# Kernel optimization log

Hardware: AMD Instinct MI355X
Metric: run time of the kernel (lower is better)

Reference implementation:

```python
import jax, jax.numpy as jnp
import numpy as np

N_NODES = 50000
N_EDGES = 800000
HIDDEN = 128
NUM_LAYERS = 3
NEG_SLOPE = 0.2  # PyG GATConv default leaky_relu slope


def setup_inputs() -> dict:
    key = jax.random.key(0)
    ks = jax.random.split(key, 10)
    d = HIDDEN
    glorot = 1.0 / np.sqrt(d)
    inp = {
        "x": jax.random.normal(ks[0], (N_NODES, d), dtype=jnp.float32),
        "edge_index": jax.random.randint(ks[1], (2, N_EDGES), 0, N_NODES, dtype=jnp.int32),
        "edge_mask": jax.random.uniform(ks[2], (N_EDGES,), dtype=jnp.float32),
        # GATConv params (heads=1)
        "W_gat": jax.random.normal(ks[3], (d, d), dtype=jnp.float32) * glorot,
        "a_src": jax.random.normal(ks[4], (d,), dtype=jnp.float32) * glorot,
        "a_dst": jax.random.normal(ks[5], (d,), dtype=jnp.float32) * glorot,
        "b_gat": jnp.zeros((d,), dtype=jnp.float32),
        # Stacked GCNConv params
        "W_gcn": jax.random.normal(ks[6], (NUM_LAYERS, d, d), dtype=jnp.float32) * glorot,
        "b_gcn": jnp.zeros((NUM_LAYERS, d), dtype=jnp.float32),
    }
    return inp


def _seg_softmax(e, seg, n):
    m = jax.ops.segment_max(e, seg, num_segments=n)
    p = jnp.exp(e - m[seg])
    s = jax.ops.segment_sum(p, seg, num_segments=n)
    return p / s[seg]


def reference(x, edge_index, edge_mask, W_gat, a_src, a_dst, b_gat, W_gcn, b_gcn):
    N = x.shape[0]
    loops = jnp.arange(N, dtype=edge_index.dtype)
    src = jnp.concatenate([edge_index[0], loops])  # [E+N] with self loops
    dst = jnp.concatenate([edge_index[1], loops])

    # --- GATConv (heads=1, add_self_loops=True); edge_attr ignored (edge_dim=None) ---
    xp = x @ W_gat                                      # [N, d]
    e = jax.nn.leaky_relu((xp @ a_src)[src] + (xp @ a_dst)[dst], NEG_SLOPE)
    alpha = _seg_softmax(e, dst, N)                     # segment softmax over incoming edges
    h = jax.ops.segment_sum(alpha[:, None] * xp[src], dst, num_segments=N) + b_gat

    # --- GCN normalization with edge_mask as edge_weight (self-loop weight = 1) ---
    w = jnp.concatenate([edge_mask, jnp.ones((N,), dtype=edge_mask.dtype)])
    deg = jax.ops.segment_sum(w, dst, num_segments=N)
    dinv = jnp.where(deg > 0, jax.lax.rsqrt(jnp.maximum(deg, 1e-12)), 0.0)
    norm = dinv[src] * w * dinv[dst]                    # [E+N]

    outs = [h]
    for l in range(NUM_LAYERS):
        z = outs[-1] @ W_gcn[l]                         # [N, d]
        z = jax.ops.segment_sum(norm[:, None] * z[src], dst, num_segments=N) + b_gcn[l]
        outs.append(jax.nn.relu(z))

    # JumpingKnowledge 'max': elementwise max over layer outputs
    return jnp.max(jnp.stack(outs, axis=0), axis=0)
```

## Files before the change

kernel.cpp:

```cpp
#include <hip/hip_runtime.h>

#define HIDDEN 128
#define NEG_SLOPE 0.2f
#define P_SORT 256

typedef unsigned short ushort_t;
typedef __attribute__((ext_vector_type(8))) short short8;
typedef __attribute__((ext_vector_type(4))) float floatx4;

static inline size_t align_up(size_t x, size_t a){ return (x + a - 1) & ~(a - 1); }

__device__ __forceinline__ ushort_t f2b(float f){
  unsigned u = __float_as_uint(f);
  unsigned r = (u + 0x7FFFu + ((u >> 16) & 1u)) >> 16;
  return (ushort_t)r;
}

__device__ __forceinline__ void fma8(float* acc, uint4 v, float a){
  acc[0] += a * __uint_as_float(v.x << 16);
  acc[1] += a * __uint_as_float(v.x & 0xFFFF0000u);
  acc[2] += a * __uint_as_float(v.y << 16);
  acc[3] += a * __uint_as_float(v.y & 0xFFFF0000u);
  acc[4] += a * __uint_as_float(v.z << 16);
  acc[5] += a * __uint_as_float(v.z & 0xFFFF0000u);
  acc[6] += a * __uint_as_float(v.w << 16);
  acc[7] += a * __uint_as_float(v.w & 0xFFFF0000u);
}

__device__ __forceinline__ uint4 pack8(const float* f){
  uint4 u;
  u.x = (unsigned)f2b(f[0]) | ((unsigned)f2b(f[1]) << 16);
  u.y = (unsigned)f2b(f[2]) | ((unsigned)f2b(f[3]) << 16);
  u.z = (unsigned)f2b(f[4]) | ((unsigned)f2b(f[5]) << 16);
  u.w = (unsigned)f2b(f[6]) | ((unsigned)f2b(f[7]) << 16);
  return u;
}


__global__ __launch_bounds__(256) void k_b1cnt(const int* __restrict__ dst,
                                               int* __restrict__ bcnt,
                                               int E, int epb, int nbkt){
  __shared__ unsigned c[256];
  int t = threadIdx.x;
  c[t] = 0;
  __syncthreads();
  int e0 = blockIdx.x * epb;
  int e1 = min(E, e0 + epb);
  for (int e = e0 + t; e < e1; e += 256) atomicAdd(&c[dst[e] >> 8], 1u);
  __syncthreads();
  if (t < nbkt) bcnt[t * P_SORT + blockIdx.x] = (int)c[t];
}

__global__ void k_scan1(const int* __restrict__ in, int* __restrict__ incl,
                        int* __restrict__ blockSums, int M){
  __shared__ int sd[256];
  int t = threadIdx.x;
  int i = blockIdx.x*256 + t;
  int v = (i < M) ? in[i] : 0;
  sd[t] = v; __syncthreads();
  for (int off = 1; off < 256; off <<= 1){
    int add = (t >= off) ? sd[t-off] : 0;
    __syncthreads();
    sd[t] += add;
    __syncthreads();
  }
  if (i < M) incl[i] = sd[t];
  if (t == 255) blockSums[blockIdx.x] = sd[255];
}

__global__ void k_scan2(const int* __restrict__ blockSums, int* __restrict__ blockOffs, int nb){
  __shared__ int sd[256];
  __shared__ int carry;
  int t = threadIdx.x;
  if (t == 0) carry = 0;
  __syncthreads();
  for (int base = 0; base < nb; base += 256){
    int i = base + t;
    int v = (i < nb) ? blockSums[i] : 0;
    sd[t] = v; __syncthreads();
    for (int off = 1; off < 256; off <<= 1){
      int add = (t >= off) ? sd[t-off] : 0;
      __syncthreads();
      sd[t] += add;
      __syncthreads();
    }
    if (i < nb) blockOffs[i] = carry + sd[t] - v;
    __syncthreads();
    if (t == 0) carry += sd[255];
    __syncthreads();
  }
}

__global__ __launch_bounds__(256) void k_b1place(const int* __restrict__ src,
                                                 const int* __restrict__ dst,
                                                 const float* __restrict__ w,
                                                 const int* __restrict__ incl,
                                                 const int* __restrict__ bcnt,
                                                 const int* __restrict__ blockOffs,
                                                 int2* __restrict__ tpw,
                                                 int E, int epb, int nbkt){
  __shared__ int base_[256];
  __shared__ unsigned c[256];
  int t = threadIdx.x;
  c[t] = 0;
  if (t < nbkt){
    int idx = t * P_SORT + blockIdx.x;
    base_[t] = incl[idx] - bcnt[idx] + blockOffs[t];
  }
  __syncthreads();
  int e0 = blockIdx.x * epb;
  int e1 = min(E, e0 + epb);
  for (int e = e0 + t; e < e1; e += 256){
    int d = dst[e];
    int b = d >> 8;
    unsigned r = atomicAdd(&c[b], 1u);
    int pos = base_[b] + (int)r;
    tpw[pos] = make_int2((int)((unsigned)src[e] | ((unsigned)(d & 255) << 16)),
                         __float_as_int(w[e]));
  }
}

__global__ __launch_bounds__(256) void k_b2(const int2* __restrict__ tpw,
                                            const int* __restrict__ blockOffs,
                                            int2* __restrict__ col_sw,
                                            int* __restrict__ rowp,
                                            float* __restrict__ dinv,
                                            int N, int E, int nbkt){
  __shared__ unsigned hcnt[256];
  __shared__ int sd[256];
  __shared__ int lofs[256];
  __shared__ unsigned rcnt[256];
  __shared__ float wsum[256];
  int b = blockIdx.x, t = threadIdx.x;
  int e0 = blockOffs[b];
  int e1 = (b + 1 < nbkt) ? blockOffs[b + 1] : E;
  hcnt[t] = 0; rcnt[t] = 0; wsum[t] = 0.f;
  __syncthreads();
  for (int e = e0 + t; e < e1; e += 256)
    atomicAdd(&hcnt[((unsigned)tpw[e].x >> 16) & 255u], 1u);
  __syncthreads();
  int v = (int)hcnt[t];
  sd[t] = v; __syncthreads();
  for (int off = 1; off < 256; off <<= 1){
    int add = (t >= off) ? sd[t-off] : 0;
    __syncthreads();
    sd[t] += add;
    __syncthreads();
  }
  lofs[t] = sd[t] - v;
  int node = b*256 + t;
  if (node < N) rowp[node] = e0 + sd[t] - v;
  if (b == 0 && t == 0) rowp[N] = E;
  __syncthreads();
  for (int e = e0 + t; e < e1; e += 256){
    int2 pw = tpw[e];
    unsigned dl = ((unsigned)pw.x >> 16) & 255u;
    unsigned r = atomicAdd(&rcnt[dl], 1u);
    int pos = e0 + lofs[dl] + (int)r;
    col_sw[pos] = make_int2((int)((unsigned)pw.x & 0xFFFFu), pw.y);
    atomicAdd(&wsum[dl], __int_as_float(pw.y));
  }
  __syncthreads();
  if (node < N) dinv[node] = rsqrtf(wsum[t] + 1.0f);
}


__global__ void k_cast_w(const float* __restrict__ Wg, const float* __restrict__ Wc,
                         ushort_t* __restrict__ Wt){
  int i = blockIdx.x*256 + threadIdx.x;
  int mat = i >> 14, idx = i & 16383;
  int k = idx >> 7, n = idx & 127;
  float v = (mat == 0) ? Wg[idx] : Wc[(mat-1)*16384 + idx];
  Wt[mat*16384 + n*128 + k] = f2b(v);
}

template<int DOTS>
__global__ __launch_bounds__(256) void k_gemm(const void* __restrict__ Ain,
                                              const ushort_t* __restrict__ Wt,
                                              ushort_t* __restrict__ C,
                                              const float* __restrict__ a_src,
                                              const float* __restrict__ a_dst,
                                              const float* __restrict__ dinv,
                                              float2* __restrict__ attr,
                                              float* __restrict__ sdst, int M){
  int wave = threadIdx.x >> 6, l = threadIdx.x & 63;
  int q = l >> 4, lm = l & 15;
  int rowBase = blockIdx.x*128 + wave*32;
  floatx4 acc[2][8];
  #pragma unroll
  for (int mt = 0; mt < 2; mt++)
    #pragma unroll
    for (int nt = 0; nt < 8; nt++) acc[mt][nt] = (floatx4){0.f,0.f,0.f,0.f};

  #pragma unroll
  for (int kc = 0; kc < 4; kc++){
    int k0 = kc*32 + q*8;
    short8 a[2];
    #pragma unroll
    for (int mt = 0; mt < 2; mt++){
      long r = rowBase + mt*16 + lm;
      if (r < M){
        if (DOTS){
          const float* ap = (const float*)Ain + r*128 + k0;
          float4 u = *(const float4*)ap;
          float4 v = *(const float4*)(ap + 4);
          short8 tv;
          tv[0]=(short)f2b(u.x); tv[1]=(short)f2b(u.y); tv[2]=(short)f2b(u.z); tv[3]=(short)f2b(u.w);
          tv[4]=(short)f2b(v.x); tv[5]=(short)f2b(v.y); tv[6]=(short)f2b(v.z); tv[7]=(short)f2b(v.w);
          a[mt] = tv;
        } else {
          a[mt] = *(const short8*)((const ushort_t*)Ain + r*128 + k0);
        }
      } else a[mt] = (short8){0,0,0,0,0,0,0,0};
    }
    #pragma unroll
    for (int nt = 0; nt < 8; nt++){
      short8 b = *(const short8*)(Wt + (nt*16 + lm)*128 + k0);
      acc[0][nt] = __builtin_amdgcn_mfma_f32_16x16x32_bf16(a[0], b, acc[0][nt], 0, 0, 0);
      acc[1][nt] = __builtin_amdgcn_mfma_f32_16x16x32_bf16(a[1], b, acc[1][nt], 0, 0, 0);
    }
  }
  #pragma unroll
  for (int mt = 0; mt < 2; mt++){
    #pragma unroll
    for (int r = 0; r < 4; r++){
      long row = rowBase + mt*16 + q*4 + r;
      if (row < M){
        #pragma unroll
        for (int nt = 0; nt < 8; nt++)
          C[row*128 + nt*16 + lm] = f2b(acc[mt][nt][r]);
      }
    }
  }
  if (DOTS){
    float as8[8], ad8[8];
    #pragma unroll
    for (int nt = 0; nt < 8; nt++){ as8[nt] = a_src[nt*16 + lm]; ad8[nt] = a_dst[nt*16 + lm]; }
    #pragma unroll
    for (int mt = 0; mt < 2; mt++){
      #pragma unroll
      for (int r = 0; r < 4; r++){
        float ps = 0.f, pd = 0.f;
        #pragma unroll
        for (int nt = 0; nt < 8; nt++){
          ps += acc[mt][nt][r] * as8[nt];
          pd += acc[mt][nt][r] * ad8[nt];
        }
        #pragma unroll
        for (int off = 1; off <= 8; off <<= 1){
          ps += __shfl_xor(ps, off, 64);
          pd += __shfl_xor(pd, off, 64);
        }
        long row = rowBase + mt*16 + q*4 + r;
        if (lm == 0 && row < M){
          attr[row] = make_float2(ps, dinv[row]);
          sdst[row] = pd;
        }
      }
    }
  }
}

template<int MODE>
__global__ __launch_bounds__(256) void k_agg(const ushort_t* __restrict__ feat,
                                             const int* __restrict__ rowp,
                                             const int2* __restrict__ col_sw,
                                             int2* __restrict__ col_en,
                                             int2* __restrict__ col_ea,
                                             const float2* __restrict__ attr,
                                             const float* __restrict__ sdst_,
                                             const float* __restrict__ dinv,
                                             const float* __restrict__ bias,
                                             ushort_t* __restrict__ out,
                                             const uint4* __restrict__ j0,
                                             const uint4* __restrict__ j1,
                                             const uint4* __restrict__ j2,
                                             float4* __restrict__ yout, int N){
  int n = blockIdx.x*4 + (threadIdx.x >> 6);
  if (n >= N) return;
  int l = threadIdx.x & 63;
  int rs = rowp[n], re = rowp[n+1];
  float inv = 0.f, pself = 0.f;
  if (MODE == 0){
    float2 an = attr[n];
    float sdd = sdst_[n];
    float es = an.x + sdd;
    es = (es >= 0.f) ? es : NEG_SLOPE*es;
    pself = __expf(es);
    float ps = 0.f;
    for (int j = rs + l; j < re; j += 64){
      int2 sw = col_sw[j];
      float w = __int_as_float(sw.y);
      float2 a = attr[sw.x];
      col_en[j] = make_int2(sw.x, __float_as_int(a.y * w * an.y));
      float ee = a.x + sdd;
      ee = (ee >= 0.f) ? ee : NEG_SLOPE*ee;
      float pe = __expf(ee);
      ps += pe;
      col_ea[j] = make_int2(sw.x, __float_as_int(pe));
    }
    #pragma unroll
    for (int off = 32; off >= 1; off >>= 1) ps += __shfl_xor(ps, off, 64);
    inv = 1.f / (ps + pself);
  }
  const int2* col = (MODE == 0) ? (const int2*)col_ea : (const int2*)col_en;
  int sub = l >> 4, q = l & 15;
  const uint4* f16 = (const uint4*)feat;
  float acc[8] = {0.f,0.f,0.f,0.f,0.f,0.f,0.f,0.f};
  for (int base = rs; base < re; base += 24){
    int2 p[6]; float a[6];
    #pragma unroll
    for (int j = 0; j < 6; j++){
      int e = base + sub + 4*j;
      int cc = min(e, re-1);
      p[j] = col[cc];
      a[j] = (e < re) ? __int_as_float(p[j].y) : 0.f;
    }
    uint4 v[6];
    #pragma unroll
    for (int j = 0; j < 6; j++) v[j] = f16[(size_t)p[j].x*16 + q];
    #pragma unroll
    for (int j = 0; j < 6; j++) fma8(acc, v[j], a[j]);
  }
  #pragma unroll
  for (int j = 0; j < 8; j++){
    acc[j] += __shfl_xor(acc[j], 16, 64);
    acc[j] += __shfl_xor(acc[j], 32, 64);
  }
  if (sub == 0){
    float sc;
    if (MODE == 0){
      #pragma unroll
      for (int j = 0; j < 8; j++) acc[j] *= inv;
      sc = pself * inv;
    } else {
      float di = dinv[n];
      sc = di * di;
    }
    uint4 v = f16[(size_t)n*16 + q];
    fma8(acc, v, sc);
    float4 b0 = ((const float4*)bias)[q*2];
    float4 b1 = ((const float4*)bias)[q*2 + 1];
    acc[0]+=b0.x; acc[1]+=b0.y; acc[2]+=b0.z; acc[3]+=b0.w;
    acc[4]+=b1.x; acc[5]+=b1.y; acc[6]+=b1.z; acc[7]+=b1.w;
    if (MODE >= 1){
      #pragma unroll
      for (int j = 0; j < 8; j++) acc[j] = fmaxf(acc[j], 0.f);
    }
    if (MODE <= 1){
      ((uint4*)out)[(size_t)n*16 + q] = pack8(acc);
    } else {
      size_t qi = (size_t)n*16 + q;
      uint4 a0 = j0[qi], a1 = j1[qi], a2 = j2[qi];
      float m[8];
      #pragma unroll
      for (int k = 0; k < 4; k++){
        unsigned u0 = (&a0.x)[k], u1 = (&a1.x)[k], u2 = (&a2.x)[k];
        float lo = fmaxf(fmaxf(__uint_as_float(u0 << 16), __uint_as_float(u1 << 16)),
                         __uint_as_float(u2 << 16));
        float hi = fmaxf(fmaxf(__uint_as_float(u0 & 0xFFFF0000u), __uint_as_float(u1 & 0xFFFF0000u)),
                         __uint_as_float(u2 & 0xFFFF0000u));
        m[k*2]   = fmaxf(acc[k*2],   lo);
        m[k*2+1] = fmaxf(acc[k*2+1], hi);
      }
      size_t yi = (size_t)n*32 + q*2;
      yout[yi]   = make_float4(m[0], m[1], m[2], m[3]);
      yout[yi+1] = make_float4(m[4], m[5], m[6], m[7]);
    }
  }
}

extern "C" void kernel_launch(void* const* d_in, const int* in_sizes, int n_in,
                              void* d_out, int out_size, void* d_ws, size_t ws_size,
                              hipStream_t stream){
  const float* x      = (const float*)d_in[0];
  const int*   eidx   = (const int*)d_in[1];
  const float* emask  = (const float*)d_in[2];
  const float* W_gat  = (const float*)d_in[3];
  const float* a_src  = (const float*)d_in[4];
  const float* a_dst  = (const float*)d_in[5];
  const float* b_gat  = (const float*)d_in[6];
  const float* W_gcn  = (const float*)d_in[7];
  const float* b_gcn  = (const float*)d_in[8];
  int N = in_sizes[0] / HIDDEN;
  int E = in_sizes[1] / 2;
  const int* src = eidx;
  const int* dst = eidx + E;

  char* p = (char*)d_ws;
  auto carve = [&](size_t bytes)->char*{ char* q = p; p += align_up(bytes, 512); return q; };
  ushort_t* zb   = (ushort_t*)carve((size_t)N*HIDDEN*2);
  ushort_t* h0   = (ushort_t*)carve((size_t)N*HIDDEN*2);
  ushort_t* h1   = (ushort_t*)carve((size_t)N*HIDDEN*2);
  ushort_t* h2   = (ushort_t*)carve((size_t)N*HIDDEN*2);
  ushort_t* Wt   = (ushort_t*)carve((size_t)4*HIDDEN*HIDDEN*2);
  float2* attr   = (float2*)carve((size_t)N*8);
  float* sdst    = (float*)carve((size_t)N*4);
  float* dinv    = (float*)carve((size_t)N*4);
  int*   rowp    = (int*)  carve((size_t)(N+1)*4);
  int2*  col_sw  = (int2*) carve((size_t)E*8);
  int2*  col_en  = (int2*) carve((size_t)E*8);
  int2*  col_ea  = (int2*) carve((size_t)E*8);
  int2*  tpw     = (int2*) carve((size_t)E*8);
  int nbkt = (N + 255) >> 8;
  int M    = nbkt * P_SORT;
  int*   bcnt  = (int*)carve((size_t)M*4);
  int*   incl  = (int*)carve((size_t)M*4);
  int nbs = (M + 255) / 256;
  int*   blockSums = (int*)carve((size_t)nbs*4);
  int*   blockOffs = (int*)carve((size_t)nbs*4);
  (void)ws_size; (void)n_in; (void)out_size;

  int epb = (E + P_SORT - 1) / P_SORT;
  int gb  = (N + 127) / 128;
  int nwb = (N + 3) / 4;

  k_b1cnt  <<<P_SORT, 256, 0, stream>>>(dst, bcnt, E, epb, nbkt);
  k_scan1  <<<nbs, 256, 0, stream>>>(bcnt, incl, blockSums, M);
  k_scan2  <<<1,   256, 0, stream>>>(blockSums, blockOffs, nbs);
  k_b1place<<<P_SORT, 256, 0, stream>>>(src, dst, emask, incl, bcnt, blockOffs,
                                        tpw, E, epb, nbkt);
  k_b2     <<<nbkt, 256, 0, stream>>>(tpw, blockOffs, col_sw, rowp, dinv, N, E, nbkt);

  k_cast_w<<<(4*HIDDEN*HIDDEN)/256, 256, 0, stream>>>(W_gat, W_gcn, Wt);

  k_gemm<1><<<gb, 256, 0, stream>>>((const void*)x, Wt, zb, a_src, a_dst, dinv, attr, sdst, N);

  k_agg<0><<<nwb, 256, 0, stream>>>(zb, rowp, col_sw, col_en, col_ea, attr, sdst,
                                    dinv, b_gat, h0, nullptr, nullptr, nullptr, nullptr, N);

  ushort_t* hs[3] = {h0, h1, h2};
  for (int l = 0; l < 2; l++){
    k_gemm<0><<<gb, 256, 0, stream>>>((const void*)hs[l], Wt + (size_t)(l+1)*HIDDEN*HIDDEN,
                                      zb, a_src, a_dst, dinv, attr, sdst, N);
    k_agg<1><<<nwb, 256, 0, stream>>>(zb, rowp, col_sw, col_en, col_ea, attr, sdst,
                                      dinv, b_gcn + (size_t)l*HIDDEN, hs[l+1],
                                      nullptr, nullptr, nullptr, nullptr, N);
  }
  k_gemm<0><<<gb, 256, 0, stream>>>((const void*)h2, Wt + (size_t)3*HIDDEN*HIDDEN,
                                    zb, a_src, a_dst, dinv, attr, sdst, N);
  k_agg<2><<<nwb, 256, 0, stream>>>(zb, rowp, col_sw, col_en, col_ea, attr, sdst,
                                    dinv, b_gcn + (size_t)2*HIDDEN, nullptr,
                                    (const uint4*)h0, (const uint4*)h1, (const uint4*)h2,
                                    (float4*)d_out, N);
}
```

Baseline: 341.7 us.

## Split edge-softmax into bucket kernel and column-chunk the aggregation grid

Moves GAT edge-score computation out of the layer-0 aggregation into a separate per-bucket kernel that accumulates softmax denominators in shared memory and writes per-node self weights. The aggregation kernels are re-gridded so each block handles one quarter of the feature columns (32 features) for 8 nodes, with 8 edges in flight per half-wave. This spreads gathered rows across four blocks, which may improve cache locality per block and occupancy. Streaming edge lists and outputs now use nontemporal loads and stores. The cost is one extra launch, and each edge list is read four times, once per column chunk.

```diff
diff --git a/kernel.cpp b/kernel.cpp
--- a/kernel.cpp
+++ b/kernel.cpp
@@ -7,6 +7,8 @@
 typedef unsigned short ushort_t;
 typedef __attribute__((ext_vector_type(8))) short short8;
 typedef __attribute__((ext_vector_type(4))) float floatx4;
+typedef __attribute__((ext_vector_type(2))) int intx2;
+typedef __attribute__((ext_vector_type(4))) unsigned uintx4;
 
 static inline size_t align_up(size_t x, size_t a){ return (x + a - 1) & ~(a - 1); }
 
@@ -34,6 +36,27 @@
   u.z = (unsigned)f2b(f[4]) | ((unsigned)f2b(f[5]) << 16);
   u.w = (unsigned)f2b(f[6]) | ((unsigned)f2b(f[7]) << 16);
   return u;
+}
+
+__device__ __forceinline__ int2 ntload2(const int2* p){
+  intx2 v = __builtin_nontemporal_load((const intx2*)p);
+  return make_int2(v.x, v.y);
+}
+__device__ __forceinline__ uint4 ntload4(const uint4* p){
+  uintx4 v = __builtin_nontemporal_load((const uintx4*)p);
+  uint4 r; r.x = v.x; r.y = v.y; r.z = v.z; r.w = v.w; return r;
+}
+__device__ __forceinline__ void ntstore2(int2* p, int2 v){
+  intx2 u; u.x = v.x; u.y = v.y;
+  __builtin_nontemporal_store(u, (intx2*)p);
+}
+__device__ __forceinline__ void ntstore4(uint4* p, uint4 v){
+  uintx4 u; u.x = v.x; u.y = v.y; u.z = v.z; u.w = v.w;
+  __builtin_nontemporal_store(u, (uintx4*)p);
+}
+__device__ __forceinline__ void ntstoref4(float4* p, float a, float b, float c, float d){
+  floatx4 u; u.x = a; u.y = b; u.z = c; u.w = d;
+  __builtin_nontemporal_store(u, (floatx4*)p);
 }
 
 
@@ -157,7 +180,7 @@
     unsigned dl = ((unsigned)pw.x >> 16) & 255u;
     unsigned r = atomicAdd(&rcnt[dl], 1u);
     int pos = e0 + lofs[dl] + (int)r;
-    col_sw[pos] = make_int2((int)((unsigned)pw.x & 0xFFFFu), pw.y);
+    col_sw[pos] = make_int2(pw.x, pw.y);
     atomicAdd(&wsum[dl], __int_as_float(pw.y));
   }
   __syncthreads();
@@ -261,97 +284,120 @@
   }
 }
 
+__global__ __launch_bounds__(256) void k_edge(const int2* __restrict__ col_sw,
+                                              const int* __restrict__ blockOffs,
+                                              const float2* __restrict__ attr,
+                                              const float* __restrict__ sdst_,
+                                              int2* __restrict__ col_en,
+                                              int2* __restrict__ col_ea,
+                                              float2* __restrict__ selfw,
+                                              int N, int E, int nbkt){
+  __shared__ float lps[256];
+  __shared__ float2 lattr[256];
+  __shared__ float lsd[256];
+  int b = blockIdx.x, t = threadIdx.x;
+  int n = b*256 + t;
+  lps[t] = 0.f;
+  if (n < N){ lattr[t] = attr[n]; lsd[t] = sdst_[n]; }
+  else { lattr[t] = make_float2(0.f, 0.f); lsd[t] = 0.f; }
+  __syncthreads();
+  int e0 = blockOffs[b];
+  int e1 = (b + 1 < nbkt) ? blockOffs[b + 1] : E;
+  for (int e = e0 + t; e < e1; e += 256){
+    int2 sw = ntload2(&col_sw[e]);
+    int src = sw.x & 0xFFFF;
+    int dl  = ((unsigned)sw.x) >> 16;
+    float w = __int_as_float(sw.y);
+    float2 a = attr[src];
+    float ee = a.x + lsd[dl];
+    ee = (ee >= 0.f) ? ee : NEG_SLOPE*ee;
+    float pe = __expf(ee);
+    atomicAdd(&lps[dl], pe);
+    ntstore2(&col_ea[e], make_int2(src, __float_as_int(pe)));
+    ntstore2(&col_en[e], make_int2(src, __float_as_int(a.y * w * lattr[dl].y)));
+  }
+  __syncthreads();
+  if (n < N){
+    float es = lattr[t].x + lsd[t];
+    es = (es >= 0.f) ? es : NEG_SLOPE*es;
+    float pself = __expf(es);
+    float inv = 1.f / (lps[t] + pself);
+    selfw[n] = make_float2(inv, pself*inv);
+  }
+}
+
 template<int MODE>
-__global__ __launch_bounds__(256) void k_agg(const ushort_t* __restrict__ feat,
-                                             const int* __restrict__ rowp,
-                                             const int2* __restrict__ col_sw,
-                                             int2* __restrict__ col_en,
-                                             int2* __restrict__ col_ea,
-                                             const float2* __restrict__ attr,
-                                             const float* __restrict__ sdst_,
-                                             const float* __restrict__ dinv,
-                                             const float* __restrict__ bias,
-                                             ushort_t* __restrict__ out,
-                                             const uint4* __restrict__ j0,
-                                             const uint4* __restrict__ j1,
-                                             const uint4* __restrict__ j2,
-                                             float4* __restrict__ yout, int N){
-  int n = blockIdx.x*4 + (threadIdx.x >> 6);
-  if (n >= N) return;
-  int l = threadIdx.x & 63;
-  int rs = rowp[n], re = rowp[n+1];
-  float inv = 0.f, pself = 0.f;
-  if (MODE == 0){
-    float2 an = attr[n];
-    float sdd = sdst_[n];
-    float es = an.x + sdd;
-    es = (es >= 0.f) ? es : NEG_SLOPE*es;
-    pself = __expf(es);
-    float ps = 0.f;
-    for (int j = rs + l; j < re; j += 64){
-      int2 sw = col_sw[j];
-      float w = __int_as_float(sw.y);
-      float2 a = attr[sw.x];
-      col_en[j] = make_int2(sw.x, __float_as_int(a.y * w * an.y));
-      float ee = a.x + sdd;
-      ee = (ee >= 0.f) ? ee : NEG_SLOPE*ee;
-      float pe = __expf(ee);
-      ps += pe;
-      col_ea[j] = make_int2(sw.x, __float_as_int(pe));
-    }
-    #pragma unroll
-    for (int off = 32; off >= 1; off >>= 1) ps += __shfl_xor(ps, off, 64);
-    inv = 1.f / (ps + pself);
-  }
-  const int2* col = (MODE == 0) ? (const int2*)col_ea : (const int2*)col_en;
-  int sub = l >> 4, q = l & 15;
+__global__ __launch_bounds__(256) void k_aggc(const ushort_t* __restrict__ feat,
+                                              const int* __restrict__ rowp,
+                                              const int2* __restrict__ col,
+                                              const float2* __restrict__ selfw,
+                                              const float* __restrict__ dinv,
+                                              const float* __restrict__ bias,
+                                              ushort_t* __restrict__ out,
+                                              const uint4* __restrict__ j0,
+                                              const uint4* __restrict__ j1,
+                                              const uint4* __restrict__ j2,
+                                              float4* __restrict__ yout, int N){
+  int bid = blockIdx.x;
+  int c = bid & 3;
+  int g = bid >> 2;
+  int wave = threadIdx.x >> 6, l = threadIdx.x & 63;
+  int half = l >> 5;
+  int n = g*8 + wave*2 + half;
+  int s = (l >> 2) & 7;
+  int q = l & 3;
   const uint4* f16 = (const uint4*)feat;
   float acc[8] = {0.f,0.f,0.f,0.f,0.f,0.f,0.f,0.f};
+  int rs = 0, re = 0;
+  if (n < N){ rs = rowp[n]; re = rowp[n+1]; }
   for (int base = rs; base < re; base += 24){
-    int2 p[6]; float a[6];
-    #pragma unroll
-    for (int j = 0; j < 6; j++){
-      int e = base + sub + 4*j;
+    int2 p[3]; float a[3];
+    #pragma unroll
+    for (int j = 0; j < 3; j++){
+      int e = base + s + 8*j;
       int cc = min(e, re-1);
-      p[j] = col[cc];
+      p[j] = ntload2(&col[cc]);
       a[j] = (e < re) ? __int_as_float(p[j].y) : 0.f;
     }
-    uint4 v[6];
-    #pragma unroll
-    for (int j = 0; j < 6; j++) v[j] = f16[(size_t)p[j].x*16 + q];
-    #pragma unroll
-    for (int j = 0; j < 6; j++) fma8(acc, v[j], a[j]);
+    uint4 v[3];
+    #pragma unroll
+    for (int j = 0; j < 3; j++) v[j] = f16[(size_t)p[j].x*16 + c*4 + q];
+    #pragma unroll
+    for (int j = 0; j < 3; j++) fma8(acc, v[j], a[j]);
   }
   #pragma unroll
   for (int j = 0; j < 8; j++){
+    acc[j] += __shfl_xor(acc[j], 4, 64);
+    acc[j] += __shfl_xor(acc[j], 8, 64);
     acc[j] += __shfl_xor(acc[j], 16, 64);
-    acc[j] += __shfl_xor(acc[j], 32, 64);
-  }
-  if (sub == 0){
+  }
+  if (s == 0 && n < N){
     float sc;
     if (MODE == 0){
+      float2 sv = selfw[n];
       #pragma unroll
-      for (int j = 0; j < 8; j++) acc[j] *= inv;
-      sc = pself * inv;
+      for (int j = 0; j < 8; j++) acc[j] *= sv.x;
+      sc = sv.y;
     } else {
       float di = dinv[n];
       sc = di * di;
     }
-    uint4 v = f16[(size_t)n*16 + q];
+    uint4 v = f16[(size_t)n*16 + c*4 + q];
     fma8(acc, v, sc);
-    float4 b0 = ((const float4*)bias)[q*2];
-    float4 b1 = ((const float4*)bias)[q*2 + 1];
+    const float4* bp = (const float4*)(bias + c*32 + q*8);
+    float4 b0 = bp[0];
+    float4 b1 = bp[1];
     acc[0]+=b0.x; acc[1]+=b0.y; acc[2]+=b0.z; acc[3]+=b0.w;
     acc[4]+=b1.x; acc[5]+=b1.y; acc[6]+=b1.z; acc[7]+=b1.w;
     if (MODE >= 1){
       #pragma unroll
       for (int j = 0; j < 8; j++) acc[j] = fmaxf(acc[j], 0.f);
     }
+    size_t qi = (size_t)n*16 + c*4 + q;
     if (MODE <= 1){
-      ((uint4*)out)[(size_t)n*16 + q] = pack8(acc);
+      ntstore4((uint4*)out + qi, pack8(acc));
     } else {
-      size_t qi = (size_t)n*16 + q;
-      uint4 a0 = j0[qi], a1 = j1[qi], a2 = j2[qi];
+      uint4 a0 = ntload4(&j0[qi]), a1 = ntload4(&j1[qi]), a2 = ntload4(&j2[qi]);
       float m[8];
       #pragma unroll
       for (int k = 0; k < 4; k++){
@@ -363,9 +409,9 @@
         m[k*2]   = fmaxf(acc[k*2],   lo);
         m[k*2+1] = fmaxf(acc[k*2+1], hi);
       }
-      size_t yi = (size_t)n*32 + q*2;
-      yout[yi]   = make_float4(m[0], m[1], m[2], m[3]);
-      yout[yi+1] = make_float4(m[4], m[5], m[6], m[7]);
+      size_t yi = (size_t)n*32 + (size_t)(c*4 + q)*2;
+      ntstoref4(&yout[yi],   m[0], m[1], m[2], m[3]);
+      ntstoref4(&yout[yi+1], m[4], m[5], m[6], m[7]);
     }
   }
 }
@@ -397,6 +443,7 @@
   float2* attr   = (float2*)carve((size_t)N*8);
   float* sdst    = (float*)carve((size_t)N*4);
   float* dinv    = (float*)carve((size_t)N*4);
+  float2* selfw  = (float2*)carve((size_t)N*8);
   int*   rowp    = (int*)  carve((size_t)(N+1)*4);
   int2*  col_sw  = (int2*) carve((size_t)E*8);
   int2*  col_en  = (int2*) carve((size_t)E*8);
@@ -413,7 +460,8 @@
 
   int epb = (E + P_SORT - 1) / P_SORT;
   int gb  = (N + 127) / 128;
-  int nwb = (N + 3) / 4;
+  int nwb2 = (N + 7) / 8;
+  int gagg = nwb2 * 4;
 
   k_b1cnt  <<<P_SORT, 256, 0, stream>>>(dst, bcnt, E, epb, nbkt);
   k_scan1  <<<nbs, 256, 0, stream>>>(bcnt, incl, blockSums, M);
@@ -426,21 +474,24 @@
 
   k_gemm<1><<<gb, 256, 0, stream>>>((const void*)x, Wt, zb, a_src, a_dst, dinv, attr, sdst, N);
 
-  k_agg<0><<<nwb, 256, 0, stream>>>(zb, rowp, col_sw, col_en, col_ea, attr, sdst,
-                                    dinv, b_gat, h0, nullptr, nullptr, nullptr, nullptr, N);
+  k_edge<<<nbkt, 256, 0, stream>>>(col_sw, blockOffs, attr, sdst, col_en, col_ea,
+                                   selfw, N, E, nbkt);
+
+  k_aggc<0><<<gagg, 256, 0, stream>>>(zb, rowp, col_ea, selfw, dinv, b_gat, h0,
+                                      nullptr, nullptr, nullptr, nullptr, N);
 
   ushort_t* hs[3] = {h0, h1, h2};
   for (int l = 0; l < 2; l++){
     k_gemm<0><<<gb, 256, 0, stream>>>((const void*)hs[l], Wt + (size_t)(l+1)*HIDDEN*HIDDEN,
                                       zb, a_src, a_dst, dinv, attr, sdst, N);
-    k_agg<1><<<nwb, 256, 0, stream>>>(zb, rowp, col_sw, col_en, col_ea, attr, sdst,
-                                      dinv, b_gcn + (size_t)l*HIDDEN, hs[l+1],
-                                      nullptr, nullptr, nullptr, nullptr, N);
+    k_aggc<1><<<gagg, 256, 0, stream>>>(zb, rowp, col_en, selfw, dinv,
+                                        b_gcn + (size_t)l*HIDDEN, hs[l+1],
+                                        nullptr, nullptr, nullptr, nullptr, N);
   }
   k_gemm<0><<<gb, 256, 0, stream>>>((const void*)h2, Wt + (size_t)3*HIDDEN*HIDDEN,
                                     zb, a_src, a_dst, dinv, attr, sdst, N);
-  k_agg<2><<<nwb, 256, 0, stream>>>(zb, rowp, col_sw, col_en, col_ea, attr, sdst,
-                                    dinv, b_gcn + (size_t)2*HIDDEN, nullptr,
-                                    (const uint4*)h0, (const uint4*)h1, (const uint4*)h2,
-                                    (float4*)d_out, N);
-}
+  k_aggc<2><<<gagg, 256, 0, stream>>>(zb, rowp, col_en, selfw, dinv,
+                                      b_gcn + (size_t)2*HIDDEN, nullptr,
+                                      (const uint4*)h0, (const uint4*)h1, (const uint4*)h2,
+                                      (float4*)d_out, N);
+}
```

Result: slower. 435.4 us (+27.4%).
